# Kernel tuning notes

Measured on AMD Instinct MI355X. Metric: run time of the kernel, lower is better.

## Reference

```python
import jax, jax.numpy as jnp
import numpy as np

B, S = 128, 256
BERT_DIM, HID, LATENT = 768, 512, 128
V = 4096        # size of valid-token id universe (valid_ids_set ~= arange(V))
K = 100         # n_clusters
VOCAB = 30522   # bow.shape[1]


def setup_inputs() -> dict:
    key = jax.random.key(0)
    ks = jax.random.split(key, 16)
    f = jnp.float32
    s = 0.02
    return {
        "input_ids": jax.random.randint(ks[0], (B, S), 0, V),
        "valid_pos": jnp.ones((B, S), jnp.int32),
        "attention_mask": jnp.ones((B, S), jnp.int32),
        "token_embs": jax.random.normal(ks[1], (B, S, BERT_DIM), f),
        "bow": jax.random.randint(ks[2], (B, VOCAB), 0, 2).astype(f),
        "enc_w1": jax.random.normal(ks[3], (BERT_DIM, HID), f) * s,
        "enc_b1": jnp.zeros((HID,), f),
        "enc_w2": jax.random.normal(ks[4], (HID, LATENT), f) * s,
        "enc_b2": jnp.zeros((LATENT,), f),
        "dec_w1": jax.random.normal(ks[5], (LATENT, HID), f) * s,
        "dec_b1": jnp.zeros((HID,), f),
        "dec_w2": jax.random.normal(ks[6], (HID, BERT_DIM), f) * s,
        "dec_b2": jnp.zeros((BERT_DIM,), f),
        "centers": jax.random.normal(ks[7], (K, LATENT), f),
        "counts": jnp.full((K,), 50.0, f),
        "vocab_weights": jax.random.uniform(ks[8], (VOCAB,), f),
    }


def reference(input_ids, valid_pos, attention_mask, token_embs, bow,
              enc_w1, enc_b1, enc_w2, enc_b2,
              dec_w1, dec_b1, dec_w2, dec_b2,
              centers, counts, vocab_weights):
    # valid_pos is all-ones -> valid_mask selects every token; flatten [B,S,D] -> [N,D]
    x = token_embs.reshape(-1, BERT_DIM)
    # AutoEncoder: encode, L2-normalize latent, decode
    h = jax.nn.relu(x @ enc_w1 + enc_b1)
    z = h @ enc_w2 + enc_b2
    z = z / jnp.linalg.norm(z, axis=-1, keepdims=True)          # latent_embs [N,LATENT]
    rec = jax.nn.relu(z @ dec_w1 + dec_b1) @ dec_w2 + dec_b2    # bert_embs_rec [N,768]
    # segment mean over unique token ids (valid_ids_set == arange(V))
    ids = input_ids.reshape(-1)
    seg_sum = jax.ops.segment_sum(z, ids, num_segments=V)
    freq = jax.ops.segment_sum(jnp.ones_like(ids, jnp.float32), ids, num_segments=V)
    avg = seg_sum / jnp.maximum(freq, 1.0)[:, None]             # avg_latent_embs [V,LATENT]
    # co-occurrence matrix: trans_matrix gathers bow columns at valid ids (= first V cols)
    nz = (bow[:, :V] != 0).astype(jnp.float32)                  # [B,V]
    p_i = nz.sum(axis=0) / B
    p_ij = (nz.T @ nz) / B                                      # [V,V]
    co_matrix = p_ij / p_i[:, None] / p_i[None, :]
    # soft k-means assignment: normalized centers, matmul, softmax, argmax
    cn = centers / jnp.linalg.norm(centers, axis=-1, keepdims=True)
    probs = jax.nn.softmax(avg @ cn.T, axis=-1)                 # [V,K]
    cluster_ids = jnp.argmax(probs, axis=1)
    # sequential EMA centroid update (equivalent ordering to per-cluster python loops;
    # clusters are independent so a single scan in sample order matches the original)
    w = vocab_weights[:V]
    valid = (freq > 0).astype(jnp.float32)                      # skip ids never seen

    def step(carry, inp):
        c, cnt = carry
        xi, ki, wi, vi = inp
        new_cnt = cnt[ki] + vi
        cnt = cnt.at[ki].set(new_cnt)
        eta = jnp.where(vi > 0, wi / new_cnt, 0.0)
        c = c.at[ki].set((1.0 - eta) * c[ki] + eta * xi)
        return (c, cnt), None

    (new_centers, _), _ = jax.lax.scan(step, (centers, counts), (avg, cluster_ids, w, valid))
    return co_matrix, rec, avg, cluster_ids, new_centers
```

## Files before the change

### kernel.cpp

```cpp
#include <hip/hip_runtime.h>
#include <cstdint>

#define M_TOK 32768
#define BERT  768
#define HID   512
#define LAT   128
#define NV    4096
#define NK    100
#define VOCAB 30522
#define NB    128

typedef short short8 __attribute__((ext_vector_type(8)));
typedef float floatx4 __attribute__((ext_vector_type(4)));
typedef unsigned short u16x4 __attribute__((ext_vector_type(4)));

__device__ __forceinline__ unsigned short f2bf(float f) {
    unsigned u = __float_as_uint(f);
    unsigned r = (u + 0x7FFFu + ((u >> 16) & 1u)) >> 16;
    return (unsigned short)r;
}
__device__ __forceinline__ float bf2f(unsigned short h) {
    return __uint_as_float((unsigned)h << 16);
}

__device__ __forceinline__ void async16(const void* g, void* l) {
    __builtin_amdgcn_global_load_lds(
        (const __attribute__((address_space(1))) unsigned int*)g,
        (__attribute__((address_space(3))) unsigned int*)l, 16, 0, 0);
}

__global__ __launch_bounds__(256) void wsplit(
    const float* __restrict__ W, unsigned short* __restrict__ Wt,
    int K, int N)
{
    int j = blockIdx.x * 256 + threadIdx.x;
    int total = N * K;
    if (j >= total) return;
    int n = j / K, k = j - n * K;
    float v = W[(size_t)k * N + n];
    unsigned short h = f2bf(v);
    float r = v - bf2f(h);
    unsigned short m = f2bf(r);
    float r2 = r - bf2f(m);
    unsigned short l = f2bf(r2);
    Wt[j] = h;
    Wt[(size_t)total + j] = m;
    Wt[(size_t)2 * total + j] = l;
}

__global__ __launch_bounds__(256) void asplit(
    const float* __restrict__ A, unsigned short* __restrict__ P, int total)
{
    int j = (blockIdx.x * 256 + threadIdx.x) * 4;
    if (j >= total) return;
    float4 v4 = *(const float4*)(A + j);
    float vv[4] = {v4.x, v4.y, v4.z, v4.w};
    u16x4 h4, m4, l4;
#pragma unroll
    for (int e = 0; e < 4; ++e) {
        float v = vv[e];
        unsigned short h = f2bf(v);
        float r = v - bf2f(h);
        unsigned short m = f2bf(r);
        float r2 = r - bf2f(m);
        h4[e] = h; m4[e] = m; l4[e] = f2bf(r2);
    }
    *(u16x4*)(P + j) = h4;
    *(u16x4*)(P + (size_t)total + j) = m4;
    *(u16x4*)(P + (size_t)2 * total + j) = l4;
}

template<int NL, bool RELU, int OUT = 0>
__global__ __launch_bounds__(256) void gemm_mfma(
    const float* __restrict__ A, const unsigned short* __restrict__ Wt,
    const float* __restrict__ bias, float* __restrict__ C,
    int M, int N, int K)
{
    __shared__ unsigned short Ash[NL][128 * 32];
    __shared__ unsigned short Bsh[NL][128 * 32];

    const int tid  = threadIdx.x;
    const int lane = tid & 63;
    const int wave = tid >> 6;
    const int bm = blockIdx.y * 128;
    const int bn = blockIdx.x * 128;
    const int wm = (wave & 1) * 64;
    const int wn = (wave >> 1) * 64;

    const int ar = tid >> 3;
    const int ak = (tid & 7) * 4;
    const int br = tid >> 2;
    const int bk = (tid & 3) * 8;

    floatx4 acc[4][4];
#pragma unroll
    for (int t = 0; t < 4; ++t)
#pragma unroll
        for (int u = 0; u < 4; ++u)
            acc[t][u] = (floatx4)0.0f;

    float4 av[4];
#pragma unroll
    for (int i = 0; i < 4; ++i)
        av[i] = *(const float4*)(A + (size_t)(bm + ar + 32 * i) * K + ak);

    for (int k0 = 0; k0 < K; k0 += 32) {
        u16x4 ah[NL][4];
#pragma unroll
        for (int i = 0; i < 4; ++i) {
            float vv[4] = {av[i].x, av[i].y, av[i].z, av[i].w};
#pragma unroll
            for (int e = 0; e < 4; ++e) {
                float v = vv[e];
                unsigned short h = f2bf(v);
                float r = v - bf2f(h);
                unsigned short m = f2bf(r);
                ah[0][i][e] = h;
                ah[1][i][e] = m;
                if (NL == 3) {
                    float r2 = r - bf2f(m);
                    ah[2][i][e] = f2bf(r2);
                }
            }
        }
        __syncthreads();
#pragma unroll
        for (int l = 0; l < NL; ++l) {
            const unsigned short* wp = Wt + (size_t)l * N * K;
#pragma unroll
            for (int i = 0; i < 2; ++i)
                async16(wp + (size_t)(bn + br + 64 * i) * K + k0 + bk,
                        &Bsh[l][i * 2048 + tid * 8]);
        }
#pragma unroll
        for (int l = 0; l < NL; ++l)
#pragma unroll
            for (int i = 0; i < 4; ++i)
                *(u16x4*)&Ash[l][(ar + 32 * i) * 32 + ak] = ah[l][i];
        if (k0 + 32 < K) {
#pragma unroll
            for (int i = 0; i < 4; ++i)
                av[i] = *(const float4*)(A + (size_t)(bm + ar + 32 * i) * K + k0 + 32 + ak);
        }
        __syncthreads();

        short8 af[NL][4];
#pragma unroll
        for (int l = 0; l < NL; ++l)
#pragma unroll
            for (int t = 0; t < 4; ++t)
                af[l][t] = *(const short8*)&Ash[l][(wm + t * 16 + (lane & 15)) * 32 + (lane >> 4) * 8];

#pragma unroll
        for (int bl = 0; bl < NL; ++bl) {
            short8 bf[4];
#pragma unroll
            for (int u = 0; u < 4; ++u)
                bf[u] = *(const short8*)&Bsh[bl][(wn + u * 16 + (lane & 15)) * 32 + (lane >> 4) * 8];
#pragma unroll
            for (int al = 0; al < NL; ++al) {
                if (al + bl >= NL) continue;
#pragma unroll
                for (int t = 0; t < 4; ++t)
#pragma unroll
                    for (int u = 0; u < 4; ++u)
                        acc[t][u] = __builtin_amdgcn_mfma_f32_16x16x32_bf16(
                            af[al][t], bf[u], acc[t][u], 0, 0, 0);
            }
        }
    }

    unsigned short* P0 = (unsigned short*)C;
    unsigned short* P1 = P0 + (size_t)M * N;
#pragma unroll
    for (int t = 0; t < 4; ++t) {
        int row0 = bm + wm + t * 16 + (lane >> 4) * 4;
#pragma unroll
        for (int u = 0; u < 4; ++u) {
            int col = bn + wn + u * 16 + (lane & 15);
            float b = bias[col];
#pragma unroll
            for (int r = 0; r < 4; ++r) {
                float v = acc[t][u][r] + b;
                if (RELU) v = fmaxf(v, 0.f);
                if (OUT == 0) {
                    C[(size_t)(row0 + r) * N + col] = v;
                } else {
                    unsigned short hh = f2bf(v);
                    unsigned short mm = f2bf(v - bf2f(hh));
                    P0[(size_t)(row0 + r) * N + col] = hh;
                    P1[(size_t)(row0 + r) * N + col] = mm;
                }
            }
        }
    }
}

template<int NP, bool RELU>
__global__ __launch_bounds__(512, 2) void gemm8p(
    const unsigned short* __restrict__ Ap,
    const unsigned short* __restrict__ Bp,
    const float* __restrict__ bias, float* __restrict__ C,
    int M, int N, int K, int NT)
{
    __shared__ unsigned short As[2][256 * 64];
    __shared__ unsigned short Bs[2][256 * 64];

    const int tid  = threadIdx.x;
    const int lane = tid & 63;
    const int wid  = tid >> 6;
    const int wm   = (wid & 1) * 128;
    const int wn   = (wid >> 1) * 64;
    const int bm   = blockIdx.y * 256;
    const int bn   = blockIdx.x * 256;

    const int laneR = lane & 15;
    const int kgrp  = lane >> 4;
    const int swz   = lane & 7;
    const int slot0 = ((kgrp)     ^ swz) * 8;
    const int slot1 = ((4 + kgrp) ^ swz) * 8;
    const int abase = (wm + laneR) * 64;
    const int bbase = (wn + laneR) * 64;

    floatx4 acc[8][4];
#pragma unroll
    for (int m = 0; m < 8; ++m)
#pragma unroll
        for (int n = 0; n < 4; ++n) acc[m][n] = (floatx4)0.0f;

    auto decode = [&](int c, int& ki, int& al, int& bl) {
        if (NP == 6) {
            ki = c / 6; int j = c - ki * 6;
            al = j < 3 ? j : (j < 5 ? j - 3 : 0);
            bl = j < 3 ? 0 : (j < 5 ? 1 : 2);
        } else {
            ki = c / 3; int j = c - ki * 3;
            al = (j == 1); bl = (j == 2);
        }
    };

    auto stageH = [&](int mat, int half, int T) {
        int ki0, al0, bl0, ki1, al1, bl1;
        decode(2 * T, ki0, al0, bl0);
        decode(2 * T + 1, ki1, al1, bl1);
        const unsigned short *base0, *base1;
        int bro;
        unsigned short* dst;
        if (mat == 0) {
            base0 = Ap + (size_t)al0 * M * K + (size_t)ki0 * 32;
            base1 = Ap + (size_t)al1 * M * K + (size_t)ki1 * 32;
            bro = bm; dst = &As[T & 1][0];
        } else {
            base0 = Bp + (size_t)bl0 * N * K + (size_t)ki0 * 32;
            base1 = Bp + (size_t)bl1 * N * K + (size_t)ki1 * 32;
            bro = bn; dst = &Bs[T & 1][0];
        }
#pragma unroll
        for (int i = 0; i < 2; ++i) {
            int row = half * 128 + i * 64 + (tid >> 3);
            int e0  = ((tid & 7) ^ (row & 7)) * 8;
            const unsigned short* src = ((e0 & 32) ? base1 : base0)
                                        + (size_t)(bro + row) * K + (e0 & 31);
            async16(src, dst + row * 64 + (tid & 7) * 8);
        }
    };

    stageH(1, 0, 0); stageH(0, 0, 0); stageH(1, 1, 0); stageH(0, 1, 0);
    stageH(1, 0, 1); stageH(0, 0, 1);
    asm volatile("s_waitcnt vmcnt(4)" ::: "memory");
    __builtin_amdgcn_s_barrier();

    for (int t = 0; t < NT; ++t) {
        const int cb = t & 1;
        const unsigned short* Ab = &As[cb][0];
        const unsigned short* Bb = &Bs[cb][0];
        short8 af[4][2], bl_[2][2], bh_[2][2];

#pragma unroll
        for (int m = 0; m < 4; ++m) {
            af[m][0] = *(const short8*)&Ab[abase + m * 1024 + slot0];
            af[m][1] = *(const short8*)&Ab[abase + m * 1024 + slot1];
        }
#pragma unroll
        for (int n = 0; n < 2; ++n) {
            bl_[n][0] = *(const short8*)&Bb[bbase + n * 1024 + slot0];
            bl_[n][1] = *(const short8*)&Bb[bbase + n * 1024 + slot1];
        }
        if (t + 1 < NT) stageH(1, 1, t + 1);
        __builtin_amdgcn_s_barrier();
        asm volatile("s_waitcnt lgkmcnt(0)" ::: "memory");
        __builtin_amdgcn_sched_barrier(0);
        __builtin_amdgcn_s_setprio(1);
#pragma unroll
        for (int m = 0; m < 4; ++m)
#pragma unroll
            for (int n = 0; n < 2; ++n)
#pragma unroll
                for (int kk = 0; kk < 2; ++kk)
                    acc[m][n] = __builtin_amdgcn_mfma_f32_16x16x32_bf16(
                        af[m][kk], bl_[n][kk], acc[m][n], 0, 0, 0);
        __builtin_amdgcn_s_setprio(0);
        __builtin_amdgcn_s_barrier();

#pragma unroll
        for (int n = 0; n < 2; ++n) {
            bh_[n][0] = *(const short8*)&Bb[bbase + (2 + n) * 1024 + slot0];
            bh_[n][1] = *(const short8*)&Bb[bbase + (2 + n) * 1024 + slot1];
        }
        if (t + 1 < NT) stageH(0, 1, t + 1);
        __builtin_amdgcn_s_barrier();
        asm volatile("s_waitcnt lgkmcnt(0)" ::: "memory");
        __builtin_amdgcn_sched_barrier(0);
        __builtin_amdgcn_s_setprio(1);
#pragma unroll
        for (int m = 0; m < 4; ++m)
#pragma unroll
            for (int n = 0; n < 2; ++n)
#pragma unroll
                for (int kk = 0; kk < 2; ++kk)
                    acc[m][2 + n] = __builtin_amdgcn_mfma_f32_16x16x32_bf16(
                        af[m][kk], bh_[n][kk], acc[m][2 + n], 0, 0, 0);
        __builtin_amdgcn_s_setprio(0);
        __builtin_amdgcn_s_barrier();

#pragma unroll
        for (int m = 0; m < 4; ++m) {
            af[m][0] = *(const short8*)&Ab[abase + (4 + m) * 1024 + slot0];
            af[m][1] = *(const short8*)&Ab[abase + (4 + m) * 1024 + slot1];
        }
        if (t + 2 < NT) stageH(1, 0, t + 2);
        __builtin_amdgcn_s_barrier();
        asm volatile("s_waitcnt lgkmcnt(0)" ::: "memory");
        __builtin_amdgcn_sched_barrier(0);
        __builtin_amdgcn_s_setprio(1);
#pragma unroll
        for (int m = 0; m < 4; ++m)
#pragma unroll
            for (int n = 0; n < 2; ++n)
#pragma unroll
                for (int kk = 0; kk < 2; ++kk)
                    acc[4 + m][2 + n] = __builtin_amdgcn_mfma_f32_16x16x32_bf16(
                        af[m][kk], bh_[n][kk], acc[4 + m][2 + n], 0, 0, 0);
        __builtin_amdgcn_s_setprio(0);
        __builtin_amdgcn_s_barrier();

        if (t + 2 < NT) stageH(0, 0, t + 2);
        if (t + 1 < NT) {
            if (t + 2 < NT) asm volatile("s_waitcnt vmcnt(4)" ::: "memory");
            else            asm volatile("s_waitcnt vmcnt(0)" ::: "memory");
        }
        __builtin_amdgcn_s_barrier();
        __builtin_amdgcn_sched_barrier(0);
        __builtin_amdgcn_s_setprio(1);
#pragma unroll
        for (int m = 0; m < 4; ++m)
#pragma unroll
            for (int n = 0; n < 2; ++n)
#pragma unroll
                for (int kk = 0; kk < 2; ++kk)
                    acc[4 + m][n] = __builtin_amdgcn_mfma_f32_16x16x32_bf16(
                        af[m][kk], bl_[n][kk], acc[4 + m][n], 0, 0, 0);
        __builtin_amdgcn_s_setprio(0);
        __builtin_amdgcn_s_barrier();
    }

#pragma unroll
    for (int mf = 0; mf < 8; ++mf) {
        int row0 = bm + wm + mf * 16 + (lane >> 4) * 4;
#pragma unroll
        for (int nf = 0; nf < 4; ++nf) {
            int col = bn + wn + nf * 16 + (lane & 15);
            float b = bias[col];
#pragma unroll
            for (int r = 0; r < 4; ++r) {
                float v = acc[mf][nf][r] + b;
                if (RELU) v = fmaxf(v, 0.f);
                C[(size_t)(row0 + r) * N + col] = v;
            }
        }
    }
}

__global__ __launch_bounds__(64) void rownorm128(const float* __restrict__ in,
                                                 float* __restrict__ out)
{
    int row = blockIdx.x;
    int l = threadIdx.x;
    const float* p = in + (size_t)row * 128;
    float v0 = p[l], v1 = p[l + 64];
    float s = v0 * v0 + v1 * v1;
#pragma unroll
    for (int o = 32; o > 0; o >>= 1) s += __shfl_xor(s, o, 64);
    float inv = 1.0f / sqrtf(s);
    float* q = out + (size_t)row * 128;
    q[l] = v0 * inv;
    q[l + 64] = v1 * inv;
}

__global__ __launch_bounds__(128) void seg_scatter(
    const float* __restrict__ z, const int* __restrict__ ids,
    float* __restrict__ seg, float* __restrict__ freq)
{
    int row = blockIdx.x;
    int l = threadIdx.x;
    int id = ids[row];
    atomicAdd(&seg[(size_t)id * 128 + l], z[(size_t)row * 128 + l]);
    if (l == 0) atomicAdd(&freq[id], 1.0f);
}

__global__ __launch_bounds__(128) void avg_kernel(
    const float* __restrict__ seg, const float* __restrict__ freq,
    float* __restrict__ avg)
{
    int i = blockIdx.x;
    int l = threadIdx.x;
    float f = fmaxf(freq[i], 1.0f);
    avg[(size_t)i * 128 + l] = seg[(size_t)i * 128 + l] / f;
}

__global__ __launch_bounds__(128) void argmax_kernel(
    const float* __restrict__ avg, const float* __restrict__ cn,
    int* __restrict__ cids, float* __restrict__ cids_f)
{
    __shared__ float arow[128];
    __shared__ float lg[NK];
    int row = blockIdx.x;
    int t = threadIdx.x;
    arow[t] = avg[(size_t)row * 128 + t];
    __syncthreads();
    if (t < NK) {
        float d = 0.f;
        const float* c = cn + (size_t)t * 128;
#pragma unroll 8
        for (int i = 0; i < 128; ++i) d += arow[i] * c[i];
        lg[t] = d;
    }
    __syncthreads();
    if (t == 0) {
        float best = lg[0];
        int bi = 0;
        for (int k = 1; k < NK; ++k) {
            if (lg[k] > best) { best = lg[k]; bi = k; }
        }
        cids[row] = bi;
        cids_f[row] = (float)bi;
    }
}

__global__ __launch_bounds__(256) void build_masks(
    const float* __restrict__ bow, unsigned long long* __restrict__ masks,
    float* __restrict__ cnt)
{
    int j = blockIdx.x * 256 + threadIdx.x;
    if (j >= NV) return;
    unsigned long long m0 = 0, m1 = 0;
    for (int b = 0; b < 64; ++b)
        if (bow[(size_t)b * VOCAB + j] != 0.f) m0 |= 1ull << b;
    for (int b = 0; b < 64; ++b)
        if (bow[(size_t)(b + 64) * VOCAB + j] != 0.f) m1 |= 1ull << b;
    masks[2 * j] = m0;
    masks[2 * j + 1] = m1;
    cnt[j] = (float)(__popcll(m0) + __popcll(m1));
}

__global__ __launch_bounds__(256) void co_kernel(
    const unsigned long long* __restrict__ masks, const float* __restrict__ cnt,
    float* __restrict__ co)
{
    int j = blockIdx.x * 256 + threadIdx.x;
    unsigned long long m0 = masks[2 * j], m1 = masks[2 * j + 1];
    float cj = cnt[j];
    int ibase = blockIdx.y * 64;
    for (int ii = 0; ii < 64; ++ii) {
        int i = ibase + ii;
        unsigned long long a0 = masks[2 * i], a1 = masks[2 * i + 1];
        float ci = cnt[i];
        float c = (float)(__popcll(a0 & m0) + __popcll(a1 & m1));
        co[(size_t)i * NV + j] = (float)NB * c / (ci * cj);
    }
}

__global__ __launch_bounds__(128) void cluster_scan(
    const float* __restrict__ avg, const int* __restrict__ cids,
    const float* __restrict__ freq, const float* __restrict__ vw,
    const float* __restrict__ centers, const float* __restrict__ counts,
    float* __restrict__ out_centers)
{
    __shared__ int list[NV];
    __shared__ float coef[NV];
    __shared__ int tcnt[128];
    __shared__ int tot;
    __shared__ float Ptot;

    int k = blockIdx.x;
    int t = threadIdx.x;

    int base = t * (NV / 128);
    int c = 0;
    for (int s = 0; s < NV / 128; ++s) {
        int i = base + s;
        if (cids[i] == k && freq[i] > 0.f) c++;
    }
    tcnt[t] = c;
    __syncthreads();
    if (t == 0) {
        int run = 0;
        for (int x = 0; x < 128; ++x) { int v = tcnt[x]; tcnt[x] = run; run += v; }
        tot = run;
    }
    __syncthreads();
    int off = tcnt[t];
    for (int s = 0; s < NV / 128; ++s) {
        int i = base + s;
        if (cids[i] == k && freq[i] > 0.f) list[off++] = i;
    }
    __syncthreads();
    int m = tot;

    float c0 = counts[k];
    for (int j = t; j < m; j += 128)
        coef[j] = vw[list[j]] / (c0 + (float)(j + 1));
    __syncthreads();
    if (t == 0) {
        float suf = 1.f;
        for (int j = m - 1; j >= 0; --j) {
            float e = coef[j];
            coef[j] = e * suf;
            suf *= (1.f - e);
        }
        Ptot = suf;
    }
    __syncthreads();

    float accv = Ptot * centers[(size_t)k * 128 + t];
    for (int j = 0; j < m; ++j)
        accv += coef[j] * avg[(size_t)list[j] * 128 + t];
    out_centers[(size_t)k * 128 + t] = accv;
}

__global__ __launch_bounds__(64) void cn_norm(const float* __restrict__ centers,
                                              float* __restrict__ cn)
{
    int row = blockIdx.x;
    int l = threadIdx.x;
    const float* p = centers + (size_t)row * 128;
    float v0 = p[l], v1 = p[l + 64];
    float s = v0 * v0 + v1 * v1;
#pragma unroll
    for (int o = 32; o > 0; o >>= 1) s += __shfl_xor(s, o, 64);
    float inv = 1.0f / sqrtf(s);
    cn[(size_t)row * 128 + l] = v0 * inv;
    cn[(size_t)row * 128 + l + 64] = v1 * inv;
}

extern "C" void kernel_launch(void* const* d_in, const int* in_sizes, int n_in,
                              void* d_out, int out_size, void* d_ws, size_t ws_size,
                              hipStream_t stream)
{
    const int*   input_ids = (const int*)d_in[0];
    const float* token_embs = (const float*)d_in[3];
    const float* bow       = (const float*)d_in[4];
    const float* enc_w1    = (const float*)d_in[5];
    const float* enc_b1    = (const float*)d_in[6];
    const float* enc_w2    = (const float*)d_in[7];
    const float* enc_b2    = (const float*)d_in[8];
    const float* dec_w1    = (const float*)d_in[9];
    const float* dec_b1    = (const float*)d_in[10];
    const float* dec_w2    = (const float*)d_in[11];
    const float* dec_b2    = (const float*)d_in[12];
    const float* centers   = (const float*)d_in[13];
    const float* counts    = (const float*)d_in[14];
    const float* vocab_w   = (const float*)d_in[15];

    float* out = (float*)d_out;
    const size_t OFF_CO  = 0;
    const size_t OFF_REC = 16777216;
    const size_t OFF_AVG = OFF_REC + 25165824;
    const size_t OFF_CID = OFF_AVG + 524288;
    const size_t OFF_NC  = OFF_CID + 4096;

    float* h    = (float*)d_ws;
    float* z    = h + (size_t)M_TOK * HID;
    float* seg  = z + (size_t)M_TOK * LAT;
    float* freq = seg + (size_t)NV * LAT;
    float* cn   = freq + NV;
    float* cntv = cn + (size_t)NK * LAT;
    int*   cids = (int*)(cntv + NV);
    unsigned long long* masks = (unsigned long long*)(cids + NV);
    unsigned short* wt1 = (unsigned short*)(masks + 2 * NV);
    unsigned short* wt2 = wt1 + (size_t)3 * HID * BERT;
    unsigned short* wt3 = wt2 + (size_t)3 * LAT * HID;
    unsigned short* wt4 = wt3 + (size_t)3 * HID * LAT;

    unsigned short* a1p = (unsigned short*)out;

    hipMemsetAsync(seg, 0, (size_t)(NV * LAT + NV) * sizeof(float), stream);

    wsplit<<<(BERT * HID + 255) / 256, 256, 0, stream>>>(enc_w1, wt1, BERT, HID);
    wsplit<<<(HID * LAT + 255) / 256, 256, 0, stream>>>(enc_w2, wt2, HID, LAT);
    wsplit<<<(LAT * HID + 255) / 256, 256, 0, stream>>>(dec_w1, wt3, LAT, HID);
    wsplit<<<(HID * BERT + 255) / 256, 256, 0, stream>>>(dec_w2, wt4, HID, BERT);

    asplit<<<(M_TOK * BERT / 4 + 255) / 256, 256, 0, stream>>>(
        token_embs, a1p, M_TOK * BERT);

    gemm8p<6, true><<<dim3(HID / 256, M_TOK / 256), 512, 0, stream>>>(
        a1p, wt1, enc_b1, h, M_TOK, HID, BERT, 6 * BERT / 64);

    gemm_mfma<3, false><<<dim3(LAT / 128, M_TOK / 128), 256, 0, stream>>>(
        h, wt2, enc_b2, z, M_TOK, LAT, HID);
    rownorm128<<<M_TOK, 64, 0, stream>>>(z, z);

    gemm_mfma<2, true, 2><<<dim3(HID / 128, M_TOK / 128), 256, 0, stream>>>(
        z, wt3, dec_b1, h, M_TOK, HID, LAT);

    gemm8p<3, false><<<dim3(BERT / 256, M_TOK / 256), 512, 0, stream>>>(
        (const unsigned short*)h, wt4, dec_b2, out + OFF_REC,
        M_TOK, BERT, HID, 3 * HID / 64);

    seg_scatter<<<M_TOK, 128, 0, stream>>>(z, input_ids, seg, freq);
    avg_kernel<<<NV, 128, 0, stream>>>(seg, freq, out + OFF_AVG);

    cn_norm<<<NK, 64, 0, stream>>>(centers, cn);
    argmax_kernel<<<NV, 128, 0, stream>>>(out + OFF_AVG, cn, cids, out + OFF_CID);

    build_masks<<<NV / 256, 256, 0, stream>>>(bow, masks, cntv);
    co_kernel<<<dim3(NV / 256, NV / 64), 256, 0, stream>>>(masks, cntv, out + OFF_CO);

    cluster_scan<<<NK, 128, 0, stream>>>(out + OFF_AVG, cids, freq, vocab_w,
                                         centers, counts, out + OFF_NC);
}
```

Before: 791.0 us.

## Load B operand directly from global into registers and remap block order

The split-bf16 GEMM no longer stages the weight (B) tiles through shared memory. Each wave reads its B fragments straight from global memory into registers, so only A is double-buffered in LDS, which halves LDS use and drops several barriers per iteration. Block indices are also remapped so groups of 8 row-blocks sharing a column tile run together, to improve L2 reuse. The risk is that B fragments now arrive through uncoalesced 16-byte global loads whose latency is exposed inside the main loop.

```diff
diff --git a/kernel.cpp b/kernel.cpp
--- a/kernel.cpp
+++ b/kernel.cpp
@@ -197,22 +197,26 @@
 }
 
 template<int NP, bool RELU>
-__global__ __launch_bounds__(512, 2) void gemm8p(
+__global__ __launch_bounds__(512, 2) void gemm_br(
     const unsigned short* __restrict__ Ap,
     const unsigned short* __restrict__ Bp,
     const float* __restrict__ bias, float* __restrict__ C,
     int M, int N, int K, int NT)
 {
     __shared__ unsigned short As[2][256 * 64];
-    __shared__ unsigned short Bs[2][256 * 64];
 
     const int tid  = threadIdx.x;
     const int lane = tid & 63;
     const int wid  = tid >> 6;
     const int wm   = (wid & 1) * 128;
     const int wn   = (wid >> 1) * 64;
-    const int bm   = blockIdx.y * 256;
-    const int bn   = blockIdx.x * 256;
+
+    const int gx = gridDim.x;
+    const int id = blockIdx.x + gx * blockIdx.y;
+    const int bxp = (id >> 3) % gx;
+    const int byp = (id & 7) + 8 * (id / (8 * gx));
+    const int bm  = byp * 256;
+    const int bn  = bxp * 256;
 
     const int laneR = lane & 15;
     const int kgrp  = lane >> 4;
@@ -220,7 +224,12 @@
     const int slot0 = ((kgrp)     ^ swz) * 8;
     const int slot1 = ((4 + kgrp) ^ swz) * 8;
     const int abase = (wm + laneR) * 64;
-    const int bbase = (wn + laneR) * 64;
+
+    unsigned rowOff[4];
+#pragma unroll
+    for (int nf = 0; nf < 4; ++nf)
+        rowOff[nf] = (unsigned)(bn + wn + nf * 16 + laneR) * (unsigned)K
+                   + (unsigned)(kgrp * 8);
 
     floatx4 acc[8][4];
 #pragma unroll
@@ -239,79 +248,84 @@
         }
     };
 
-    auto stageH = [&](int mat, int half, int T) {
+    auto stageA = [&](int T) {
         int ki0, al0, bl0, ki1, al1, bl1;
         decode(2 * T, ki0, al0, bl0);
         decode(2 * T + 1, ki1, al1, bl1);
-        const unsigned short *base0, *base1;
-        int bro;
-        unsigned short* dst;
-        if (mat == 0) {
-            base0 = Ap + (size_t)al0 * M * K + (size_t)ki0 * 32;
-            base1 = Ap + (size_t)al1 * M * K + (size_t)ki1 * 32;
-            bro = bm; dst = &As[T & 1][0];
-        } else {
-            base0 = Bp + (size_t)bl0 * N * K + (size_t)ki0 * 32;
-            base1 = Bp + (size_t)bl1 * N * K + (size_t)ki1 * 32;
-            bro = bn; dst = &Bs[T & 1][0];
-        }
-#pragma unroll
-        for (int i = 0; i < 2; ++i) {
-            int row = half * 128 + i * 64 + (tid >> 3);
-            int e0  = ((tid & 7) ^ (row & 7)) * 8;
-            const unsigned short* src = ((e0 & 32) ? base1 : base0)
-                                        + (size_t)(bro + row) * K + (e0 & 31);
+        const unsigned short* A0 = Ap + (size_t)al0 * M * K + (size_t)ki0 * 32;
+        const unsigned short* A1 = Ap + (size_t)al1 * M * K + (size_t)ki1 * 32;
+        unsigned short* dst = &As[T & 1][0];
+#pragma unroll
+        for (int i = 0; i < 4; ++i) {
+            int s   = i * 512 + tid;
+            int row = s >> 3;
+            int e0  = ((s & 7) ^ (row & 7)) * 8;
+            const unsigned short* src = ((e0 & 32) ? A1 : A0)
+                                        + (size_t)(bm + row) * K + (e0 & 31);
             async16(src, dst + row * 64 + (tid & 7) * 8);
         }
     };
 
-    stageH(1, 0, 0); stageH(0, 0, 0); stageH(1, 1, 0); stageH(0, 1, 0);
-    stageH(1, 0, 1); stageH(0, 0, 1);
-    asm volatile("s_waitcnt vmcnt(4)" ::: "memory");
+    stageA(0);
+    asm volatile("s_waitcnt vmcnt(0)" ::: "memory");
     __builtin_amdgcn_s_barrier();
 
     for (int t = 0; t < NT; ++t) {
         const int cb = t & 1;
         const unsigned short* Ab = &As[cb][0];
-        const unsigned short* Bb = &Bs[cb][0];
-        short8 af[4][2], bl_[2][2], bh_[2][2];
-
-#pragma unroll
-        for (int m = 0; m < 4; ++m) {
-            af[m][0] = *(const short8*)&Ab[abase + m * 1024 + slot0];
-            af[m][1] = *(const short8*)&Ab[abase + m * 1024 + slot1];
-        }
-#pragma unroll
-        for (int n = 0; n < 2; ++n) {
-            bl_[n][0] = *(const short8*)&Bb[bbase + n * 1024 + slot0];
-            bl_[n][1] = *(const short8*)&Bb[bbase + n * 1024 + slot1];
-        }
-        if (t + 1 < NT) stageH(1, 1, t + 1);
-        __builtin_amdgcn_s_barrier();
-        asm volatile("s_waitcnt lgkmcnt(0)" ::: "memory");
+        short8 af[4][2], b[4][2];
+
+        af[0][0] = *(const short8*)&Ab[abase + 0 * 1024 + slot0];
+        af[0][1] = *(const short8*)&Ab[abase + 0 * 1024 + slot1];
+        af[1][0] = *(const short8*)&Ab[abase + 1 * 1024 + slot0];
+        af[1][1] = *(const short8*)&Ab[abase + 1 * 1024 + slot1];
+        __builtin_amdgcn_sched_barrier(0);
+        af[2][0] = *(const short8*)&Ab[abase + 2 * 1024 + slot0];
+        af[2][1] = *(const short8*)&Ab[abase + 2 * 1024 + slot1];
+        af[3][0] = *(const short8*)&Ab[abase + 3 * 1024 + slot0];
+        af[3][1] = *(const short8*)&Ab[abase + 3 * 1024 + slot1];
+        __builtin_amdgcn_sched_barrier(0);
+
+        int ki0, al0, bl0, ki1, al1, bl1;
+        decode(2 * t, ki0, al0, bl0);
+        decode(2 * t + 1, ki1, al1, bl1);
+        const unsigned short* B0 = Bp + (size_t)bl0 * N * K + (size_t)ki0 * 32;
+        const unsigned short* B1 = Bp + (size_t)bl1 * N * K + (size_t)ki1 * 32;
+#pragma unroll
+        for (int nf = 0; nf < 4; ++nf) {
+            b[nf][0] = *(const short8*)(B0 + rowOff[nf]);
+            b[nf][1] = *(const short8*)(B1 + rowOff[nf]);
+        }
+        __builtin_amdgcn_sched_barrier(0);
+        if (t + 1 < NT) stageA(t + 1);
+        __builtin_amdgcn_sched_barrier(0);
+
+        asm volatile("s_waitcnt lgkmcnt(4)" ::: "memory");
+        if (t + 1 < NT) asm volatile("s_waitcnt vmcnt(4)" ::: "memory");
+        else            asm volatile("s_waitcnt vmcnt(0)" ::: "memory");
         __builtin_amdgcn_sched_barrier(0);
         __builtin_amdgcn_s_setprio(1);
 #pragma unroll
-        for (int m = 0; m < 4; ++m)
+        for (int m = 0; m < 2; ++m)
 #pragma unroll
             for (int n = 0; n < 2; ++n)
 #pragma unroll
                 for (int kk = 0; kk < 2; ++kk)
                     acc[m][n] = __builtin_amdgcn_mfma_f32_16x16x32_bf16(
-                        af[m][kk], bl_[n][kk], acc[m][n], 0, 0, 0);
+                        af[m][kk], b[n][kk], acc[m][n], 0, 0, 0);
         __builtin_amdgcn_s_setprio(0);
-        __builtin_amdgcn_s_barrier();
-
-#pragma unroll
-        for (int n = 0; n < 2; ++n) {
-            bh_[n][0] = *(const short8*)&Bb[bbase + (2 + n) * 1024 + slot0];
-            bh_[n][1] = *(const short8*)&Bb[bbase + (2 + n) * 1024 + slot1];
-        }
-        if (t + 1 < NT) stageH(0, 1, t + 1);
-        __builtin_amdgcn_s_barrier();
+
         asm volatile("s_waitcnt lgkmcnt(0)" ::: "memory");
         __builtin_amdgcn_sched_barrier(0);
         __builtin_amdgcn_s_setprio(1);
+#pragma unroll
+        for (int m = 2; m < 4; ++m)
+#pragma unroll
+            for (int n = 0; n < 2; ++n)
+#pragma unroll
+                for (int kk = 0; kk < 2; ++kk)
+                    acc[m][n] = __builtin_amdgcn_mfma_f32_16x16x32_bf16(
+                        af[m][kk], b[n][kk], acc[m][n], 0, 0, 0);
 #pragma unroll
         for (int m = 0; m < 4; ++m)
 #pragma unroll
@@ -319,17 +333,18 @@
 #pragma unroll
                 for (int kk = 0; kk < 2; ++kk)
                     acc[m][2 + n] = __builtin_amdgcn_mfma_f32_16x16x32_bf16(
-                        af[m][kk], bh_[n][kk], acc[m][2 + n], 0, 0, 0);
+                        af[m][kk], b[2 + n][kk], acc[m][2 + n], 0, 0, 0);
         __builtin_amdgcn_s_setprio(0);
-        __builtin_amdgcn_s_barrier();
-
-#pragma unroll
-        for (int m = 0; m < 4; ++m) {
-            af[m][0] = *(const short8*)&Ab[abase + (4 + m) * 1024 + slot0];
-            af[m][1] = *(const short8*)&Ab[abase + (4 + m) * 1024 + slot1];
-        }
-        if (t + 2 < NT) stageH(1, 0, t + 2);
-        __builtin_amdgcn_s_barrier();
+        __builtin_amdgcn_sched_barrier(0);
+
+        af[0][0] = *(const short8*)&Ab[abase + 4 * 1024 + slot0];
+        af[0][1] = *(const short8*)&Ab[abase + 4 * 1024 + slot1];
+        af[1][0] = *(const short8*)&Ab[abase + 5 * 1024 + slot0];
+        af[1][1] = *(const short8*)&Ab[abase + 5 * 1024 + slot1];
+        af[2][0] = *(const short8*)&Ab[abase + 6 * 1024 + slot0];
+        af[2][1] = *(const short8*)&Ab[abase + 6 * 1024 + slot1];
+        af[3][0] = *(const short8*)&Ab[abase + 7 * 1024 + slot0];
+        af[3][1] = *(const short8*)&Ab[abase + 7 * 1024 + slot1];
         asm volatile("s_waitcnt lgkmcnt(0)" ::: "memory");
         __builtin_amdgcn_sched_barrier(0);
         __builtin_amdgcn_s_setprio(1);
@@ -340,18 +355,7 @@
 #pragma unroll
                 for (int kk = 0; kk < 2; ++kk)
                     acc[4 + m][2 + n] = __builtin_amdgcn_mfma_f32_16x16x32_bf16(
-                        af[m][kk], bh_[n][kk], acc[4 + m][2 + n], 0, 0, 0);
-        __builtin_amdgcn_s_setprio(0);
-        __builtin_amdgcn_s_barrier();
-
-        if (t + 2 < NT) stageH(0, 0, t + 2);
-        if (t + 1 < NT) {
-            if (t + 2 < NT) asm volatile("s_waitcnt vmcnt(4)" ::: "memory");
-            else            asm volatile("s_waitcnt vmcnt(0)" ::: "memory");
-        }
-        __builtin_amdgcn_s_barrier();
-        __builtin_amdgcn_sched_barrier(0);
-        __builtin_amdgcn_s_setprio(1);
+                        af[m][kk], b[2 + n][kk], acc[4 + m][2 + n], 0, 0, 0);
 #pragma unroll
         for (int m = 0; m < 4; ++m)
 #pragma unroll
@@ -359,8 +363,10 @@
 #pragma unroll
                 for (int kk = 0; kk < 2; ++kk)
                     acc[4 + m][n] = __builtin_amdgcn_mfma_f32_16x16x32_bf16(
-                        af[m][kk], bl_[n][kk], acc[4 + m][n], 0, 0, 0);
+                        af[m][kk], b[n][kk], acc[4 + m][n], 0, 0, 0);
         __builtin_amdgcn_s_setprio(0);
+
+        asm volatile("s_waitcnt vmcnt(0)" ::: "memory");
         __builtin_amdgcn_s_barrier();
     }
 
@@ -370,10 +376,10 @@
 #pragma unroll
         for (int nf = 0; nf < 4; ++nf) {
             int col = bn + wn + nf * 16 + (lane & 15);
-            float b = bias[col];
+            float bb = bias[col];
 #pragma unroll
             for (int r = 0; r < 4; ++r) {
-                float v = acc[mf][nf][r] + b;
+                float v = acc[mf][nf][r] + bb;
                 if (RELU) v = fmaxf(v, 0.f);
                 C[(size_t)(row0 + r) * N + col] = v;
             }
@@ -604,7 +610,7 @@
     asplit<<<(M_TOK * BERT / 4 + 255) / 256, 256, 0, stream>>>(
         token_embs, a1p, M_TOK * BERT);
 
-    gemm8p<6, true><<<dim3(HID / 256, M_TOK / 256), 512, 0, stream>>>(
+    gemm_br<6, true><<<dim3(HID / 256, M_TOK / 256), 512, 0, stream>>>(
         a1p, wt1, enc_b1, h, M_TOK, HID, BERT, 6 * BERT / 64);
 
     gemm_mfma<3, false><<<dim3(LAT / 128, M_TOK / 128), 256, 0, stream>>>(
@@ -614,7 +620,7 @@
     gemm_mfma<2, true, 2><<<dim3(HID / 128, M_TOK / 128), 256, 0, stream>>>(
         z, wt3, dec_b1, h, M_TOK, HID, LAT);
 
-    gemm8p<3, false><<<dim3(BERT / 256, M_TOK / 256), 512, 0, stream>>>(
+    gemm_br<3, false><<<dim3(BERT / 256, M_TOK / 256), 512, 0, stream>>>(
         (const unsigned short*)h, wt4, dec_b2, out + OFF_REC,
         M_TOK, BERT, HID, 3 * HID / 64);
 
```

New measurement: 900.1 us. 13.8% more time.
